# Kernel optimization log

Measured on AMD Instinct MI355X. Metric: run time of the kernel, lower is better.

Reference implementation:

```python
import jax, jax.numpy as jnp
import numpy as np

N = 50000
E = 800000
IN_DIM = 256
HID = 128
HALF = HID // 2
OUT_DIM = 2


def setup_inputs() -> dict:
    key = jax.random.key(0)
    ks = jax.random.split(key, 16)
    s = lambda fan_in: 1.0 / np.sqrt(fan_in)
    inp = {
        "x": jax.random.normal(ks[0], (N, IN_DIM), dtype=jnp.float32),
        "edge_index": jax.random.randint(ks[1], (2, E), 0, N, dtype=jnp.int64),
        # lin_in: input_dim -> hidden
        "W_in": jax.random.uniform(ks[2], (IN_DIM, HID), jnp.float32, -s(IN_DIM), s(IN_DIM)),
        "b_in": jnp.zeros((HID,), jnp.float32),
        # lin_nor / lin_abnor: half -> hidden
        "W_nor": jax.random.uniform(ks[3], (HALF, HID), jnp.float32, -s(HALF), s(HALF)),
        "b_nor": jnp.zeros((HID,), jnp.float32),
        "W_abnor": jax.random.uniform(ks[4], (HALF, HID), jnp.float32, -s(HALF), s(HALF)),
        "b_abnor": jnp.zeros((HID,), jnp.float32),
        # attention gate
        "W_att": jax.random.uniform(ks[5], (HID, HID), jnp.float32, -s(HID), s(HID)),
        "b_att": jnp.zeros((HID,), jnp.float32),
        "v_att": jax.random.uniform(ks[6], (HID, 1), jnp.float32, -s(HID), s(HID)),
        # update linear
        "W_upd": jax.random.uniform(ks[7], (HID, HID), jnp.float32, -s(HID), s(HID)),
        "b_upd": jnp.zeros((HID,), jnp.float32),
        # classifier
        "W_cls": jax.random.uniform(ks[8], (HID, OUT_DIM), jnp.float32, -s(HID), s(HID)),
        "b_cls": jnp.zeros((OUT_DIM,), jnp.float32),
    }
    return inp


def reference(x, edge_index, W_in, b_in, W_nor, b_nor, W_abnor, b_abnor,
              W_att, b_att, v_att, W_upd, b_upd, W_cls, b_cls):
    n = x.shape[0]
    # add self loops (add_self_loops)
    loops = jnp.tile(jnp.arange(n, dtype=edge_index.dtype), (2, 1))
    ei = jnp.concatenate([edge_index, loops], axis=1)
    row, col = ei[0], ei[1]  # row = source j, col = target i

    # lin_in + leaky_relu (dropout p=0 / eval)
    h = jax.nn.leaky_relu(x @ W_in + b_in)

    # split halves and project
    x_nor = h[:, :HALF] @ W_nor + b_nor      # [N, HID]
    x_abnor = h[:, HALF:] @ W_abnor + b_abnor

    # symmetric normalization by target degree
    deg = jax.ops.segment_sum(jnp.ones_like(col, dtype=h.dtype), col, num_segments=n)
    dinv = jnp.where(deg > 0, jax.lax.rsqrt(jnp.where(deg > 0, deg, 1.0)), 0.0)
    norm = dinv[row] * dinv[col]             # [E']

    # per-edge gather
    xn_j = x_nor[row]                        # [E', HID]
    xa_j = x_abnor[row]

    # denoising attention gate: sigmoid(v^T tanh(W(xn+xa)+b))
    h_att = jnp.tanh((xn_j + xa_j) @ W_att + b_att)
    alpha = jax.nn.sigmoid(h_att @ v_att)    # [E', 1]

    msg = norm[:, None] * (alpha * xn_j + (1.0 - alpha) * xa_j)

    # scatter-add to targets
    aggr = jax.ops.segment_sum(msg, col, num_segments=n)  # [N, HID]

    upd = aggr @ W_upd + b_upd
    out = jax.nn.leaky_relu(upd) @ W_cls + b_cls
    return out
```

## Files before the change

kernel.cpp:

```cpp
#include <hip/hip_runtime.h>

#define N_NODES 50000
#define E_EDGES 800000
#define IN_DIM  256
#define HID     128
#define HALF    64
#define OUT_DIM 2
#define NW      32
#define SLOPE   0.01f

#define ST      132
#define WSLICE  (NW * ST)

#define SSTRIDE 520
#define PLANE   (8 * SSTRIDE)

#define SCAN_B  512
#define SCAN_NB ((N_NODES + SCAN_B - 1) / SCAN_B)

typedef unsigned int uint32;
typedef __attribute__((ext_vector_type(8)))  __bf16 bf16x8v;
typedef __attribute__((ext_vector_type(16))) float  f32x16;

union BF8 { bf16x8v v; unsigned short s[8]; uint4 q; };

#define FI_F 0
#define FN_F 4096
#define FA_F 5120
#define FT_F 6144
#define FU_F 8192
#define F_TOTAL 10240

__device__ __forceinline__ uint32 rne16u(uint32 u) {
    return (u + 0x7fffu + ((u >> 16) & 1u)) >> 16;
}

__device__ __forceinline__ uint32 pack_hl(float v) {
    uint32 uu = __float_as_uint(v);
    uint32 hh = rne16u(uu);
    float  fh = __uint_as_float(hh << 16);
    float  r  = v - fh;
    uint32 ll = rne16u(__float_as_uint(r));
    return (hh << 16) | ll;
}

__device__ __forceinline__ float fast_tanh(float x) {
    float ex = __expf(2.f * x);
    return 1.f - 2.f * __builtin_amdgcn_rcpf(ex + 1.f);
}
__device__ __forceinline__ float fast_sig(float x) {
    return __builtin_amdgcn_rcpf(1.f + __expf(-x));
}

__device__ __forceinline__ void mfma3(f32x16& acc, bf16x8v ah, bf16x8v al,
                                      bf16x8v bh, bf16x8v bl) {
    acc = __builtin_amdgcn_mfma_f32_32x32x16_bf16(ah, bh, acc, 0, 0, 0);
    acc = __builtin_amdgcn_mfma_f32_32x32x16_bf16(ah, bl, acc, 0, 0, 0);
    acc = __builtin_amdgcn_mfma_f32_32x32x16_bf16(al, bh, acc, 0, 0, 0);
}

__device__ __forceinline__ void stage_split4(__bf16* __restrict__ Ahi,
                                             __bf16* __restrict__ Alo,
                                             int rr, int k, float4 v) {
    int s_idx = k >> 4, jb = k & 7, lt = rr + 32 * ((k >> 3) & 1);
    int base = s_idx * SSTRIDE + lt * 8 + jb;
    float f[4] = {v.x, v.y, v.z, v.w};
    uint32 h[4], lo[4];
    #pragma unroll
    for (int j = 0; j < 4; j++) {
        uint32 uu = __float_as_uint(f[j]);
        uint32 hh = rne16u(uu);
        float  fh = __uint_as_float(hh << 16);
        float  r  = f[j] - fh;
        h[j] = hh; lo[j] = rne16u(__float_as_uint(r));
    }
    *(uint2*)(Ahi + base) = make_uint2(h[0] | (h[1] << 16), h[2] | (h[3] << 16));
    *(uint2*)(Alo + base) = make_uint2(lo[0] | (lo[1] << 16), lo[2] | (lo[3] << 16));
}

__device__ __forceinline__ void mfma_gemm1_pre(f32x16& acc,
        const __bf16* __restrict__ Ahi, const __bf16* __restrict__ Alo,
        int S, int sg0, const uint4* __restrict__ F, int fbase, int l, int t) {
    for (int s = 0; s < S; s++) {
        bf16x8v ah = *(const bf16x8v*)&Ahi[s * SSTRIDE + l * 8];
        bf16x8v al = *(const bf16x8v*)&Alo[s * SSTRIDE + l * 8];
        int f = fbase + ((sg0 + s) * 4 + t) * 64 + l;
        BF8 bh, bl; bh.q = F[2 * f]; bl.q = F[2 * f + 1];
        mfma3(acc, ah, al, bh.v, bl.v);
    }
}

__device__ __forceinline__ void mfma_gemm1_pk(f32x16& acc, const uint32* T,
        int aoff, int S, const uint4* __restrict__ F, int fbase, int l, int t) {
    const int row = l & 31, khi = 8 * (l >> 5);
    for (int s = 0; s < S; s++) {
        int k0 = aoff + 16 * s + khi;
        uint4 qa = *(const uint4*)&T[row * ST + k0];
        uint4 qb = *(const uint4*)&T[row * ST + k0 + 4];
        BF8 ah, al;
        ah.q.x = (qa.x >> 16) | (qa.y & 0xffff0000u);
        ah.q.y = (qa.z >> 16) | (qa.w & 0xffff0000u);
        ah.q.z = (qb.x >> 16) | (qb.y & 0xffff0000u);
        ah.q.w = (qb.z >> 16) | (qb.w & 0xffff0000u);
        al.q.x = (qa.x & 0xffffu) | (qa.y << 16);
        al.q.y = (qa.z & 0xffffu) | (qa.w << 16);
        al.q.z = (qb.x & 0xffffu) | (qb.y << 16);
        al.q.w = (qb.z & 0xffffu) | (qb.w << 16);
        int f = fbase + (s * 4 + t) * 64 + l;
        BF8 bh, bl; bh.q = F[2 * f]; bl.q = F[2 * f + 1];
        mfma3(acc, ah.v, al.v, bh.v, bl.v);
    }
}

__device__ __forceinline__ uint32 pack_bf2(float x, float y) {
    return rne16u(__float_as_uint(x)) | (rne16u(__float_as_uint(y)) << 16);
}

__global__ void zero_int_kernel(int* __restrict__ p, int n) {
    int i = blockIdx.x * blockDim.x + threadIdx.x;
    if (i < n) p[i] = 0;
}

__global__ void deg_ticket_kernel(const int* __restrict__ col,
                                  int* __restrict__ cnt, int* __restrict__ ticket) {
    int e = blockIdx.x * blockDim.x + threadIdx.x;
    if (e < E_EDGES) ticket[e] = atomicAdd(&cnt[col[e]], 1);
}

__device__ __forceinline__ int wave_iscan(int v, int l) {
    #pragma unroll
    for (int off = 1; off < 64; off <<= 1) {
        int t = __shfl_up(v, off, 64);
        if (l >= off) v += t;
    }
    return v;
}

__global__ __launch_bounds__(SCAN_B) void scan1_kernel(
    const int* __restrict__ cnt, int* __restrict__ row_start, int* __restrict__ bsum)
{
    __shared__ int wsum[SCAN_B / 64];
    int i = blockIdx.x * SCAN_B + threadIdx.x;
    int v = (i < N_NODES) ? cnt[i] : 0;
    int l = threadIdx.x & 63, w = threadIdx.x >> 6;
    int isc = wave_iscan(v, l);
    if (l == 63) wsum[w] = isc;
    __syncthreads();
    int wo = 0;
    #pragma unroll
    for (int k = 0; k < SCAN_B / 64; k++) wo += (k < w) ? wsum[k] : 0;
    if (i < N_NODES) row_start[i] = wo + isc - v;
    if (threadIdx.x == SCAN_B - 1) bsum[blockIdx.x] = wo + isc;
}

__global__ __launch_bounds__(128) void scan2_kernel(
    int* __restrict__ bsum, int* __restrict__ row_start)
{
    __shared__ int wsum[2];
    int i = threadIdx.x;
    int v = (i < SCAN_NB) ? bsum[i] : 0;
    int l = i & 63, w = i >> 6;
    int isc = wave_iscan(v, l);
    if (l == 63) wsum[w] = isc;
    __syncthreads();
    int wo = (w == 1) ? wsum[0] : 0;
    if (i < SCAN_NB) bsum[i] = wo + isc - v;
    if (i == SCAN_NB - 1) row_start[N_NODES] = wo + isc;
}

__global__ __launch_bounds__(SCAN_B) void scan3_kernel(
    const int* __restrict__ bsum, int* __restrict__ row_start)
{
    int i = blockIdx.x * SCAN_B + threadIdx.x;
    if (i < N_NODES) row_start[i] += bsum[blockIdx.x];
}

__global__ void fill_kernel(const int* __restrict__ ei,
                            const int* __restrict__ row_start,
                            const int* __restrict__ ticket,
                            int* __restrict__ csr_src)
{
    int e = blockIdx.x * blockDim.x + threadIdx.x;
    if (e >= E_EDGES) return;
    int j = ei[e];
    int i = ei[E_EDGES + e];
    csr_src[row_start[i] + ticket[e]] = j;
}

__global__ __launch_bounds__(256) void prep_w_kernel(
    const float* __restrict__ W_in, const float* __restrict__ W_nor,
    const float* __restrict__ W_ab, const float* __restrict__ W_att,
    const float* __restrict__ W_upd,
    uint4* __restrict__ F)
{
    int idx = blockIdx.x * 256 + threadIdx.x;
    const float* W; int fbase, fi;
    if (idx < 4096)       { W = W_in;  fbase = FI_F; fi = idx; }
    else if (idx < 5120)  { W = W_nor; fbase = FN_F; fi = idx - 4096; }
    else if (idx < 6144)  { W = W_ab;  fbase = FA_F; fi = idx - 5120; }
    else if (idx < 8192)  { W = W_att; fbase = FT_F; fi = idx - 6144; }
    else if (idx < 10240) { W = W_upd; fbase = FU_F; fi = idx - 8192; }
    else return;
    int l = fi & 63, st = fi >> 6, t = st & 3, s = st >> 2;
    int k0 = 16 * s + 8 * (l >> 5);
    int c  = 32 * t + (l & 31);
    uint32 hi[8], lo[8];
    #pragma unroll
    for (int j = 0; j < 8; j++) {
        float v = W[(size_t)(k0 + j) * HID + c];
        uint32 uu = __float_as_uint(v);
        uint32 h  = rne16u(uu);
        float  fh = __uint_as_float(h << 16);
        float  r  = v - fh;
        hi[j] = h;
        lo[j] = rne16u(__float_as_uint(r));
    }
    uint4 H, L;
    H.x = hi[0] | (hi[1] << 16); H.y = hi[2] | (hi[3] << 16);
    H.z = hi[4] | (hi[5] << 16); H.w = hi[6] | (hi[7] << 16);
    L.x = lo[0] | (lo[1] << 16); L.y = lo[2] | (lo[3] << 16);
    L.z = lo[4] | (lo[5] << 16); L.w = lo[6] | (lo[7] << 16);
    int f = fbase + fi;
    F[2 * f]     = H;
    F[2 * f + 1] = L;
}

__global__ __launch_bounds__(256, 4) void node_phase_kernel(
    const float* __restrict__ x,
    const float* __restrict__ b_in,  const float* __restrict__ b_nor,
    const float* __restrict__ b_abnor, const float* __restrict__ b_att,
    const float* __restrict__ v_att,
    const int* __restrict__ cnt,
    const uint4* __restrict__ F,
    uint32* __restrict__ u)
{
    __shared__ __align__(16) float smem[WSLICE];
    __shared__ float dinvs[NW];
    __shared__ float gpart[4][NW];
    __bf16* Ahi = (__bf16*)smem;
    __bf16* Alo = (__bf16*)smem + PLANE;
    uint32* T   = (uint32*)smem;

    const int tid    = threadIdx.x;
    const int w      = tid >> 6;
    const int l      = tid & 63;
    const int col    = l & 31;
    const int hi     = l >> 5;
    const int wnode0 = blockIdx.x * NW;

    if (tid < NW) {
        int nd = wnode0 + tid;
        float c = (nd < N_NODES) ? (float)cnt[nd] : 0.f;
        dinvs[tid] = rsqrtf(c + 1.0f);
    }

    f32x16 hacc;
    {
        float bv = b_in[32 * w + col];
        #pragma unroll
        for (int r2 = 0; r2 < 16; r2++) hacc[r2] = bv;
    }
    for (int half = 0; half < 2; half++) {
        #pragma unroll
        for (int it = 0; it < 4; it++) {
            int i = it * 256 + tid;
            int rr = i >> 5, kq = i & 31, k = 4 * kq;
            int nd = wnode0 + rr; if (nd >= N_NODES) nd = N_NODES - 1;
            float4 v = *(const float4*)(x + (size_t)nd * IN_DIM + half * 128 + k);
            stage_split4(Ahi, Alo, rr, k, v);
        }
        __syncthreads();
        mfma_gemm1_pre(hacc, Ahi, Alo, 8, half * 8, F, FI_F, l, w);
        __syncthreads();
    }

    #pragma unroll
    for (int rg = 0; rg < 16; rg++) {
        int rrow = (rg & 3) + 8 * (rg >> 2) + 4 * hi;
        float v = hacc[rg];
        v = v > 0.f ? v : SLOPE * v;
        T[rrow * ST + 32 * w + col] = pack_hl(v);
    }
    __syncthreads();

    f32x16 xn, xa;
    {
        float bv = b_nor[32 * w + col];
        #pragma unroll
        for (int r2 = 0; r2 < 16; r2++) xn[r2] = bv;
    }
    mfma_gemm1_pk(xn, T, 0, 4, F, FN_F, l, w);
    {
        float bv = b_abnor[32 * w + col];
        #pragma unroll
        for (int r2 = 0; r2 < 16; r2++) xa[r2] = bv;
    }
    mfma_gemm1_pk(xa, T, HALF, 4, F, FA_F, l, w);
    __syncthreads();

    f32x16 sv, d;
    #pragma unroll
    for (int rg = 0; rg < 16; rg++) {
        int rrow = (rg & 3) + 8 * (rg >> 2) + 4 * hi;
        sv[rg] = xn[rg] + xa[rg];
        d[rg]  = xn[rg] - xa[rg];
        T[rrow * ST + 32 * w + col] = pack_hl(sv[rg]);
    }
    __syncthreads();

    f32x16 tac;
    {
        float bv = b_att[32 * w + col];
        #pragma unroll
        for (int r2 = 0; r2 < 16; r2++) tac[r2] = bv;
    }
    mfma_gemm1_pk(tac, T, 0, 8, F, FT_F, l, w);

    float g[16];
    {
        float vv = v_att[32 * w + col];
        #pragma unroll
        for (int rg = 0; rg < 16; rg++) g[rg] = fast_tanh(tac[rg]) * vv;
    }
    #pragma unroll
    for (int msk = 16; msk >= 1; msk >>= 1) {
        #pragma unroll
        for (int rg = 0; rg < 16; rg++) g[rg] += __shfl_xor(g[rg], msk, 64);
    }
    if (col == 0) {
        #pragma unroll
        for (int rg = 0; rg < 16; rg++) {
            int rrow = (rg & 3) + 8 * (rg >> 2) + 4 * hi;
            gpart[w][rrow] = g[rg];
        }
    }
    __syncthreads();

    float am[16];
    #pragma unroll
    for (int rg = 0; rg < 16; rg++) {
        int rrow = (rg & 3) + 8 * (rg >> 2) + 4 * hi;
        float gt = gpart[0][rrow] + gpart[1][rrow] + gpart[2][rrow] + gpart[3][rrow];
        am[rg] = fast_sig(gt) - 0.5f;
    }

    #pragma unroll
    for (int rg = 0; rg < 16; rg++) {
        int rrow = (rg & 3) + 8 * (rg >> 2) + 4 * hi;
        int n    = wnode0 + rrow;
        float uv = dinvs[rrow] * (0.5f * sv[rg] + am[rg] * d[rg]);
        float pv = __shfl_xor(uv, 1, 64);
        if (((l & 1) == 0) && n < N_NODES) {
            u[(size_t)n * (HID / 2) + 16 * w + (col >> 1)] = pack_bf2(uv, pv);
        }
    }
}

__global__ __launch_bounds__(256) void gather_kernel(
    const int* __restrict__ row_start, const int* __restrict__ csr_src,
    const uint32* __restrict__ u, float* __restrict__ acc)
{
    int node = blockIdx.x * 4 + (threadIdx.x >> 6);
    int lane = threadIdx.x & 63;
    if (node >= N_NODES) return;

    const size_t RW = HID / 2;
    uint32 v = u[(size_t)node * RW + lane];
    float sx = __uint_as_float(v << 16);
    float sy = __uint_as_float(v & 0xffff0000u);

    int b = row_start[node], e = row_start[node + 1];
    for (int p = b; p < e; p += 8) {
        int idx[8];
        #pragma unroll
        for (int q = 0; q < 8; q++) {
            int a = p + q; if (a > e - 1) a = e - 1;
            idx[q] = csr_src[a];
        }
        uint32 vv[8];
        #pragma unroll
        for (int q = 0; q < 8; q++) vv[q] = u[(size_t)idx[q] * RW + lane];
        #pragma unroll
        for (int q = 0; q < 8; q++) {
            if (p + q < e) {
                sx += __uint_as_float(vv[q] << 16);
                sy += __uint_as_float(vv[q] & 0xffff0000u);
            }
        }
    }
    float2 s = make_float2(sx, sy);
    *(float2*)(acc + (size_t)node * HID + lane * 2) = s;
}

__global__ __launch_bounds__(256, 4) void final_phase_kernel(
    const float* __restrict__ acc, const int* __restrict__ cnt,
    const float* __restrict__ b_upd,
    const float* __restrict__ W_cls, const float* __restrict__ b_cls,
    const uint4* __restrict__ F,
    float* __restrict__ out)
{
    __shared__ __align__(16) float smem[WSLICE];
    __bf16* Ahi = (__bf16*)smem;
    __bf16* Alo = (__bf16*)smem + PLANE;

    const int tid    = threadIdx.x;
    const int w      = tid >> 6;
    const int l      = tid & 63;
    const int col    = l & 31;
    const int hi     = l >> 5;
    const int wnode0 = blockIdx.x * NW;

    #pragma unroll
    for (int it = 0; it < 4; it++) {
        int i = it * 256 + tid;
        int rr = i >> 5, kq = i & 31, k = 4 * kq;
        int nd = wnode0 + rr; if (nd >= N_NODES) nd = N_NODES - 1;
        float dv = rsqrtf((float)cnt[nd] + 1.0f);
        float4 v = *(const float4*)(acc + (size_t)nd * HID + k);
        v.x *= dv; v.y *= dv; v.z *= dv; v.w *= dv;
        stage_split4(Ahi, Alo, rr, k, v);
    }
    __syncthreads();

    f32x16 up;
    {
        float bv = b_upd[32 * w + col];
        #pragma unroll
        for (int r2 = 0; r2 < 16; r2++) up[r2] = bv;
    }
    mfma_gemm1_pre(up, Ahi, Alo, 8, 0, F, FU_F, l, w);
    __syncthreads();

    float* B = smem;
    #pragma unroll
    for (int rg = 0; rg < 16; rg++) {
        int rrow = (rg & 3) + 8 * (rg >> 2) + 4 * hi;
        float v = up[rg];
        B[rrow * ST + 32 * w + col] = v > 0.f ? v : SLOPE * v;
    }
    __syncthreads();

    {
        int n = tid >> 3, o = (tid >> 2) & 1, c = tid & 3;
        float s = 0.f;
        int k0 = c * 32;
        for (int k = k0; k < k0 + 32; k++)
            s = fmaf(B[n * ST + k], W_cls[k * OUT_DIM + o], s);
        s += __shfl_xor(s, 1, 64);
        s += __shfl_xor(s, 2, 64);
        if (c == 0 && wnode0 + n < N_NODES) {
            out[(size_t)(wnode0 + n) * OUT_DIM + o] = s + b_cls[o];
        }
    }
}

extern "C" void kernel_launch(void* const* d_in, const int* in_sizes, int n_in,
                              void* d_out, int out_size, void* d_ws, size_t ws_size,
                              hipStream_t stream)
{
    const float* x       = (const float*)d_in[0];
    const int*   ei      = (const int*)  d_in[1];
    const float* W_in    = (const float*)d_in[2];
    const float* b_in    = (const float*)d_in[3];
    const float* W_nor   = (const float*)d_in[4];
    const float* b_nor   = (const float*)d_in[5];
    const float* W_abnor = (const float*)d_in[6];
    const float* b_abnor = (const float*)d_in[7];
    const float* W_att   = (const float*)d_in[8];
    const float* b_att   = (const float*)d_in[9];
    const float* v_att   = (const float*)d_in[10];
    const float* W_upd   = (const float*)d_in[11];
    const float* b_upd   = (const float*)d_in[12];
    const float* W_cls   = (const float*)d_in[13];
    const float* b_cls   = (const float*)d_in[14];
    float* out = (float*)d_out;

    char* base = (char*)d_ws;
    int*  cnt       = (int*)base;
    int*  row_start = cnt + N_NODES;
    int*  bsum      = row_start + (N_NODES + 1);
    int*  csr_src   = bsum + 128;
    size_t off_u    = (((size_t)(2 * N_NODES + 129 + E_EDGES)) * 4 + 63) & ~(size_t)63;
    uint32* u       = (uint32*)(base + off_u);
    size_t off_acc  = (off_u + (size_t)N_NODES * (HID / 2) * 4 + 63) & ~(size_t)63;
    float* acc      = (float*)(base + off_acc);
    int*   ticket   = (int*)acc;
    size_t off_f    = (off_acc + (size_t)N_NODES * HID * 4 + 63) & ~(size_t)63;
    uint4* F        = (uint4*)(base + off_f);

    const int nblk = (N_NODES + NW - 1) / NW;

    zero_int_kernel<<<(N_NODES + 255) / 256, 256, 0, stream>>>(cnt, N_NODES);
    deg_ticket_kernel<<<(E_EDGES + 255) / 256, 256, 0, stream>>>(ei + E_EDGES, cnt, ticket);
    scan1_kernel<<<SCAN_NB, SCAN_B, 0, stream>>>(cnt, row_start, bsum);
    scan2_kernel<<<1, 128, 0, stream>>>(bsum, row_start);
    scan3_kernel<<<SCAN_NB, SCAN_B, 0, stream>>>(bsum, row_start);
    fill_kernel<<<(E_EDGES + 255) / 256, 256, 0, stream>>>(ei, row_start, ticket, csr_src);
    prep_w_kernel<<<F_TOTAL / 256, 256, 0, stream>>>(W_in, W_nor, W_abnor, W_att, W_upd, F);
    node_phase_kernel<<<nblk, 256, 0, stream>>>(
        x, b_in, b_nor, b_abnor, b_att, v_att, cnt, F, u);
    gather_kernel<<<(N_NODES + 3) / 4, 256, 0, stream>>>(row_start, csr_src, u, acc);
    final_phase_kernel<<<nblk, 256, 0, stream>>>(
        acc, cnt, b_upd, W_cls, b_cls, F, out);
}
```

Before: 162.0 us.

## Fuse CSR neighbor gather into final phase kernel, drop acc buffer

Moves the per-node neighbor aggregation into the final GEMM kernel. Each wave now gathers 8 nodes sequentially and writes the normalized, split-bf16 results straight into shared memory, which removes the fp32 acc round trip (about 25 MB written and read) and one kernel launch. The cost is less parallelism: the gather now runs over fewer, larger blocks and processes nodes serially per wave, so memory-latency hiding may suffer. The ticket buffer gets its own workspace slot because acc no longer exists.

Result: no change. 159.9 us (-1.3%).

```diff
diff --git a/kernel.cpp b/kernel.cpp
--- a/kernel.cpp
+++ b/kernel.cpp
@@ -356,44 +356,9 @@
     }
 }
 
-__global__ __launch_bounds__(256) void gather_kernel(
+__global__ __launch_bounds__(256, 4) void final_fused_kernel(
     const int* __restrict__ row_start, const int* __restrict__ csr_src,
-    const uint32* __restrict__ u, float* __restrict__ acc)
-{
-    int node = blockIdx.x * 4 + (threadIdx.x >> 6);
-    int lane = threadIdx.x & 63;
-    if (node >= N_NODES) return;
-
-    const size_t RW = HID / 2;
-    uint32 v = u[(size_t)node * RW + lane];
-    float sx = __uint_as_float(v << 16);
-    float sy = __uint_as_float(v & 0xffff0000u);
-
-    int b = row_start[node], e = row_start[node + 1];
-    for (int p = b; p < e; p += 8) {
-        int idx[8];
-        #pragma unroll
-        for (int q = 0; q < 8; q++) {
-            int a = p + q; if (a > e - 1) a = e - 1;
-            idx[q] = csr_src[a];
-        }
-        uint32 vv[8];
-        #pragma unroll
-        for (int q = 0; q < 8; q++) vv[q] = u[(size_t)idx[q] * RW + lane];
-        #pragma unroll
-        for (int q = 0; q < 8; q++) {
-            if (p + q < e) {
-                sx += __uint_as_float(vv[q] << 16);
-                sy += __uint_as_float(vv[q] & 0xffff0000u);
-            }
-        }
-    }
-    float2 s = make_float2(sx, sy);
-    *(float2*)(acc + (size_t)node * HID + lane * 2) = s;
-}
-
-__global__ __launch_bounds__(256, 4) void final_phase_kernel(
-    const float* __restrict__ acc, const int* __restrict__ cnt,
+    const uint32* __restrict__ u, const int* __restrict__ cnt,
     const float* __restrict__ b_upd,
     const float* __restrict__ W_cls, const float* __restrict__ b_cls,
     const uint4* __restrict__ F,
@@ -410,15 +375,44 @@
     const int hi     = l >> 5;
     const int wnode0 = blockIdx.x * NW;
 
-    #pragma unroll
-    for (int it = 0; it < 4; it++) {
-        int i = it * 256 + tid;
-        int rr = i >> 5, kq = i & 31, k = 4 * kq;
+    const size_t RW = HID / 2;
+    const int kk   = 2 * l;
+    const int sidx = kk >> 4, jj = kk & 7, ltb = 32 * ((kk >> 3) & 1);
+
+    for (int q = 0; q < 8; q++) {
+        int rr = 8 * w + q;
         int nd = wnode0 + rr; if (nd >= N_NODES) nd = N_NODES - 1;
+
+        uint32 v = u[(size_t)nd * RW + l];
+        float sx = __uint_as_float(v << 16);
+        float sy = __uint_as_float(v & 0xffff0000u);
+
+        int b = row_start[nd], e = row_start[nd + 1];
+        for (int p = b; p < e; p += 8) {
+            int idx[8];
+            #pragma unroll
+            for (int qq = 0; qq < 8; qq++) {
+                int a = p + qq; if (a > e - 1) a = e - 1;
+                idx[qq] = csr_src[a];
+            }
+            uint32 vv[8];
+            #pragma unroll
+            for (int qq = 0; qq < 8; qq++) vv[qq] = u[(size_t)idx[qq] * RW + l];
+            #pragma unroll
+            for (int qq = 0; qq < 8; qq++) {
+                if (p + qq < e) {
+                    sx += __uint_as_float(vv[qq] << 16);
+                    sy += __uint_as_float(vv[qq] & 0xffff0000u);
+                }
+            }
+        }
         float dv = rsqrtf((float)cnt[nd] + 1.0f);
-        float4 v = *(const float4*)(acc + (size_t)nd * HID + k);
-        v.x *= dv; v.y *= dv; v.z *= dv; v.w *= dv;
-        stage_split4(Ahi, Alo, rr, k, v);
+        sx *= dv; sy *= dv;
+
+        uint32 px = pack_hl(sx), py = pack_hl(sy);
+        int base = sidx * SSTRIDE + (rr + ltb) * 8 + jj;
+        *(uint32*)&Ahi[base] = (px >> 16) | (py & 0xffff0000u);
+        *(uint32*)&Alo[base] = (px & 0xffffu) | (py << 16);
     }
     __syncthreads();
 
@@ -480,12 +474,10 @@
     int*  row_start = cnt + N_NODES;
     int*  bsum      = row_start + (N_NODES + 1);
     int*  csr_src   = bsum + 128;
-    size_t off_u    = (((size_t)(2 * N_NODES + 129 + E_EDGES)) * 4 + 63) & ~(size_t)63;
+    int*  ticket    = csr_src + E_EDGES;
+    size_t off_u    = (((size_t)(2 * N_NODES + 129 + 2 * E_EDGES)) * 4 + 63) & ~(size_t)63;
     uint32* u       = (uint32*)(base + off_u);
-    size_t off_acc  = (off_u + (size_t)N_NODES * (HID / 2) * 4 + 63) & ~(size_t)63;
-    float* acc      = (float*)(base + off_acc);
-    int*   ticket   = (int*)acc;
-    size_t off_f    = (off_acc + (size_t)N_NODES * HID * 4 + 63) & ~(size_t)63;
+    size_t off_f    = (off_u + (size_t)N_NODES * (HID / 2) * 4 + 63) & ~(size_t)63;
     uint4* F        = (uint4*)(base + off_f);
 
     const int nblk = (N_NODES + NW - 1) / NW;
@@ -499,7 +491,6 @@
     prep_w_kernel<<<F_TOTAL / 256, 256, 0, stream>>>(W_in, W_nor, W_abnor, W_att, W_upd, F);
     node_phase_kernel<<<nblk, 256, 0, stream>>>(
         x, b_in, b_nor, b_abnor, b_att, v_att, cnt, F, u);
-    gather_kernel<<<(N_NODES + 3) / 4, 256, 0, stream>>>(row_start, csr_src, u, acc);
-    final_phase_kernel<<<nblk, 256, 0, stream>>>(
-        acc, cnt, b_upd, W_cls, b_cls, F, out);
-}
+    final_fused_kernel<<<nblk, 256, 0, stream>>>(
+        row_start, csr_src, u, cnt, b_upd, W_cls, b_cls, F, out);
+}
```
